# Kernel optimization log

Hardware: AMD Instinct MI355X
Metric: run time of the kernel (lower is better)

## Reference

```python
import jax, jax.numpy as jnp
import numpy as np

B, S, D_IN, D_H = 16, 4096, 512, 512

def setup_inputs() -> dict:
    key = jax.random.key(0)
    ks = jax.random.split(key, 8)
    inp = {
        "input": jax.random.normal(ks[0], (B, D_IN), dtype=jnp.float32),
        "context": jax.random.normal(ks[1], (B, S, D_IN), dtype=jnp.float32),
        "mask": jax.random.bernoulli(ks[2], 0.2, (B, S)),
        # parameters (torch nn.Linear layout: W [out,in], b [out])
        "W_in": jax.random.normal(ks[3], (D_H, D_IN), dtype=jnp.float32) / np.sqrt(D_IN),
        "b_in": jax.random.normal(ks[4], (D_H,), dtype=jnp.float32) * 0.01,
        "W_ctx": jax.random.normal(ks[5], (D_H, D_IN), dtype=jnp.float32) / np.sqrt(D_IN),
        "b_ctx": jax.random.normal(ks[6], (D_H,), dtype=jnp.float32) * 0.01,
        "v": jax.random.normal(ks[7], (D_H,), dtype=jnp.float32),
    }
    return inp


def reference(input, context, mask, W_in, b_in, W_ctx, b_ctx, v):
    # inp: [B, H] projected decoder state
    inp = input @ W_in.T + b_in
    # ctx: [B, S, H] projected context (this is what the torch code matmuls
    # with the softmax weights, i.e. hidden lives in hidden_dim space)
    ctx = context @ W_ctx.T + b_ctx
    # additive (Bahdanau) scores: v . tanh(inp + ctx) -> [B, S]
    scores = jnp.einsum("h,bsh->bs", v, jnp.tanh(inp[:, None, :] + ctx))
    # masked positions get -inf so they receive zero softmax weight
    scores = jnp.where(mask, -jnp.inf, scores)
    attn = jax.nn.softmax(scores, axis=-1)  # [B, S]
    # weighted sum of projected context: [B, H]
    hidden = jnp.einsum("bsh,bs->bh", ctx, attn)
    return hidden, attn
```

## Files before the change

kernel.cpp:

```cpp
#include <hip/hip_runtime.h>
#include <hip/hip_bf16.h>

#define B_  16
#define S_  4096
#define DIN 512
#define DH  512

typedef _Float16 f16x8 __attribute__((ext_vector_type(8)));
typedef float    f32x4 __attribute__((ext_vector_type(4)));


__device__ __forceinline__ float fast_tanh(float x) {
    float e = __expf(2.f * x);
    return 1.f - 2.f * __builtin_amdgcn_rcpf(e + 1.f);
}

__device__ __forceinline__ void gload_lds16(const void* g, void* l) {
    __builtin_amdgcn_global_load_lds(
        (const __attribute__((address_space(1))) void*)g,
        (__attribute__((address_space(3))) void*)l, 16, 0, 0);
}

__device__ __forceinline__ int mask_at(const void* mask, int isByte, int idx) {
    return isByte ? (int)((const unsigned char*)mask)[idx]
                  : ((const int*)mask)[idx];
}

__global__ __launch_bounds__(256)
void prep_kernel(const float* __restrict__ input,
                 const float* __restrict__ W_in,
                 const float* __restrict__ b_in,
                 const float* __restrict__ W_ctx,
                 const float* __restrict__ b_ctx,
                 const void*  __restrict__ mask,
                 _Float16* __restrict__ W16,
                 float* __restrict__ addv,
                 float* __restrict__ wsum,
                 int* __restrict__ maskflag) {
    int blk = blockIdx.x;
    int tid = threadIdx.x;
    if (blk < 256) {
        int base = blk * 1024 + tid * 4;
        float4 wv = *(const float4*)(W_ctx + base);
        union { _Float16 f[4]; ushort4 u; } cv;
        cv.f[0] = (_Float16)wv.x; cv.f[1] = (_Float16)wv.y;
        cv.f[2] = (_Float16)wv.z; cv.f[3] = (_Float16)wv.w;
        *(ushort4*)(W16 + base) = cv.u;
    } else if (blk < 288) {
        int t = blk - 256;
        int b = t >> 1;
        int h = ((t & 1) << 8) + tid;
        __shared__ float inrow[DIN];
        inrow[tid]       = input[b * DIN + tid];
        inrow[tid + 256] = input[b * DIN + tid + 256];
        __syncthreads();
        const float* wr = W_in + (size_t)h * DIN;
        float acc = 0.f;
        for (int k = 0; k < DIN; k += 4) {
            float4 w4 = *(const float4*)(wr + k);
            acc += w4.x * inrow[k] + w4.y * inrow[k + 1]
                 + w4.z * inrow[k + 2] + w4.w * inrow[k + 3];
        }
        addv[b * DH + h] = acc + b_in[h] + b_ctx[h];
    } else if (blk == 288) {
        const uint4* m4 = (const uint4*)mask;
        unsigned int orw = 0;
#pragma unroll
        for (int it = 0; it < 16; ++it) {
            uint4 w = m4[it * 256 + tid];
            orw |= (w.x | w.y | w.z | w.w);
        }
        int found = ((orw & 0xFFFFFF00u) != 0) ? 1 : 0;
        __shared__ int f;
        if (tid == 0) f = 0;
        __syncthreads();
        if (found) atomicOr(&f, 1);
        __syncthreads();
        if (tid == 0) maskflag[0] = f;
    } else {
        int base = (blk - 289) * 4096;
#pragma unroll
        for (int it = 0; it < 16; ++it)
            wsum[base + it * 256 + tid] = 0.f;
    }
}

__global__ __launch_bounds__(512, 1)
void score_kernel(const float* __restrict__ context,
                  const _Float16* __restrict__ W16,
                  const float* __restrict__ addv,
                  const float* __restrict__ v,
                  float* __restrict__ scores) {
    __shared__ __align__(16) _Float16 As[2][4096];
    __shared__ __align__(16) _Float16 Bs[2][16384];

    const int tid  = threadIdx.x;
    const int wave = tid >> 6;
    const int lane = tid & 63;
    const int l15  = lane & 15;
    const int q    = lane >> 4;
    const int sg   = wave >> 2;
    const int ng   = wave & 3;

    const int b  = blockIdx.x >> 5;
    const int st = blockIdx.x & 31;
    const int s0 = st * 128;

    const float* ctxA = context + ((size_t)b * S_ + s0) * DIN;

    const int rowA = ((tid >> 6) * 16) + (tid & 15);
    const int kbA  = ((tid >> 4) & 3) * 8;

#define STAGE_B(kc_, buf_)                                                     \
    {                                                                          \
        _Pragma("unroll")                                                      \
        for (int u = 0; u < 4; ++u) {                                          \
            int jn = wave * 4 + u;                                             \
            const _Float16* gp = W16 +                                         \
                (size_t)(jn * 16 + l15) * DIN + (kc_) * 32 + q * 8;            \
            gload_lds16(gp, &Bs[buf_][jn * 512]);                              \
        }                                                                      \
    }

#define LOADA(kc_, set_)                                                       \
    {                                                                          \
        const float* g0 = ctxA + (size_t)rowA * DIN + (kc_) * 32 + kbA;        \
        set_[0] = *(const float4*)g0;                                          \
        set_[1] = *(const float4*)(g0 + 4);                                    \
    }

#define WRITEA(set_, buf_)                                                     \
    {                                                                          \
        f16x8 h0;                                                              \
        h0[0] = (_Float16)set_[0].x; h0[1] = (_Float16)set_[0].y;              \
        h0[2] = (_Float16)set_[0].z; h0[3] = (_Float16)set_[0].w;              \
        h0[4] = (_Float16)set_[1].x; h0[5] = (_Float16)set_[1].y;              \
        h0[6] = (_Float16)set_[1].z; h0[7] = (_Float16)set_[1].w;              \
        *(f16x8*)&As[buf_][tid * 8] = h0;                                      \
    }

    f32x4 acc[4][8];
#pragma unroll
    for (int jm = 0; jm < 4; ++jm)
#pragma unroll
        for (int jn = 0; jn < 8; ++jn) acc[jm][jn] = (f32x4){0.f, 0.f, 0.f, 0.f};

    float4 aA[2], aB[2];

    STAGE_B(0, 0);
    LOADA(0, aA);
    WRITEA(aA, 0);
    LOADA(1, aB);
    __syncthreads();

#define STEP(kc_, buf_, ldset_, wrset_)                                        \
    {                                                                          \
        if ((kc_) + 1 < 16) STAGE_B((kc_) + 1, (buf_) ^ 1);                    \
        if ((kc_) + 2 < 16) LOADA((kc_) + 2, ldset_);                          \
        f16x8 afr[4], bfr[8];                                                  \
        _Pragma("unroll")                                                      \
        for (int jm = 0; jm < 4; ++jm)                                         \
            afr[jm] = *(const f16x8*)&As[buf_][(sg * 4 + jm) * 512 +           \
                                              q * 128 + l15 * 8];              \
        _Pragma("unroll")                                                      \
        for (int jn = 0; jn < 8; ++jn)                                         \
            bfr[jn] = *(const f16x8*)&Bs[buf_][(ng * 8 + jn) * 512 +           \
                                              q * 128 + l15 * 8];              \
        _Pragma("unroll")                                                      \
        for (int jn = 0; jn < 8; ++jn)                                         \
            _Pragma("unroll")                                                  \
            for (int jm = 0; jm < 4; ++jm)                                     \
                acc[jm][jn] = __builtin_amdgcn_mfma_f32_16x16x32_f16(          \
                    afr[jm], bfr[jn], acc[jm][jn], 0, 0, 0);                   \
        if ((kc_) + 1 < 16) WRITEA(wrset_, (buf_) ^ 1);                        \
        __syncthreads();                                                       \
    }

    for (int kp = 0; kp < 8; ++kp) {
        STEP(2 * kp,     0, aA, aB);
        STEP(2 * kp + 1, 1, aB, aA);
    }

    const float* avb = addv + b * DH;
    float rowsum[4][4] = {{0.f,0.f,0.f,0.f},{0.f,0.f,0.f,0.f},
                          {0.f,0.f,0.f,0.f},{0.f,0.f,0.f,0.f}};
#pragma unroll
    for (int jn = 0; jn < 8; ++jn) {
        int n = (ng * 8 + jn) * 16 + l15;
        float av = avb[n];
        float vv = v[n];
#pragma unroll
        for (int jm = 0; jm < 4; ++jm)
#pragma unroll
            for (int r = 0; r < 4; ++r)
                rowsum[jm][r] += vv * fast_tanh(acc[jm][jn][r] + av);
    }
    float* sredF = (float*)&As[0][0];
#pragma unroll
    for (int jm = 0; jm < 4; ++jm)
#pragma unroll
        for (int r = 0; r < 4; ++r) {
            float s = rowsum[jm][r];
            s += __shfl_xor(s, 1, 16);
            s += __shfl_xor(s, 2, 16);
            s += __shfl_xor(s, 4, 16);
            s += __shfl_xor(s, 8, 16);
            if (l15 == 0) {
                int rowL = (sg * 4 + jm) * 16 + q * 4 + r;
                sredF[ng * 128 + rowL] = s;
            }
        }
    __syncthreads();
    if (tid < 128) {
        float out = sredF[tid] + sredF[128 + tid] +
                    sredF[256 + tid] + sredF[384 + tid];
        scores[b * S_ + s0 + tid] = out;
    }
}

__global__ __launch_bounds__(256)
void attnwsum_kernel(const float* __restrict__ scores,
                     const float* __restrict__ context,
                     const void* __restrict__ mask,
                     const int* __restrict__ maskflag,
                     float* __restrict__ attn,
                     float* __restrict__ wsum) {
    __shared__ float rbuf[8];
    __shared__ int   selIdx[64];
    __shared__ float selW[64];
    __shared__ int   selCount;
    __shared__ float sh[1024];

    int b  = blockIdx.x >> 6;
    int c0 = (blockIdx.x & 63) * 64;
    int tid = threadIdx.x;
    int wv = tid >> 6, ln = tid & 63;
    int isByte = maskflag[0];
    const float* sr = scores + b * S_;

    float mx = -__builtin_inff();
    float vals[16];
#pragma unroll
    for (int it = 0; it < 16; ++it) {
        int s = it * 256 + tid;
        float x = mask_at(mask, isByte, b * S_ + s) ? -__builtin_inff() : sr[s];
        vals[it] = x;
        mx = fmaxf(mx, x);
    }
    for (int o = 1; o < 64; o <<= 1) mx = fmaxf(mx, __shfl_xor(mx, o, 64));
    if (ln == 0) rbuf[wv] = mx;
    __syncthreads();
    mx = fmaxf(fmaxf(rbuf[0], rbuf[1]), fmaxf(rbuf[2], rbuf[3]));

    float sum = 0.f;
#pragma unroll
    for (int it = 0; it < 16; ++it) sum += __expf(vals[it] - mx);
    for (int o = 1; o < 64; o <<= 1) sum += __shfl_xor(sum, o, 64);
    if (ln == 0) rbuf[4 + wv] = sum;
    if (tid == 0) selCount = 0;
    __syncthreads();
    float inv = 1.f / (rbuf[4] + rbuf[5] + rbuf[6] + rbuf[7]);

    if (tid < 64) {
        int s = c0 + tid;
        int idx = b * S_ + s;
        float sc = mask_at(mask, isByte, idx) ? -__builtin_inff() : sr[s];
        float p = __expf(sc - mx) * inv;
        attn[idx] = p;
        if (p > 1e-9f) {
            int k = atomicAdd(&selCount, 1);
            selIdx[k] = s;
            selW[k]  = p;
        }
    }
    __syncthreads();

    int cnt = selCount;
    if (cnt == 0) return;

    const float* cb = context + (size_t)b * S_ * DIN;
    const int p  = tid >> 7;
    const int hb = (tid & 127) * 4;
    float4 aE = {0.f, 0.f, 0.f, 0.f};
    float4 aO = {0.f, 0.f, 0.f, 0.f};
    int i = p;
    for (; i + 2 < cnt; i += 4) {
        const float* r0 = cb + (size_t)selIdx[i]     * DIN + hb;
        const float* r1 = cb + (size_t)selIdx[i + 2] * DIN + hb;
        float w0 = selW[i], w1 = selW[i + 2];
        float4 v0 = *(const float4*)r0;
        float4 v1 = *(const float4*)r1;
        aE.x += w0 * v0.x; aE.y += w0 * v0.y; aE.z += w0 * v0.z; aE.w += w0 * v0.w;
        aO.x += w1 * v1.x; aO.y += w1 * v1.y; aO.z += w1 * v1.z; aO.w += w1 * v1.w;
    }
    for (; i < cnt; i += 2) {
        const float* r0 = cb + (size_t)selIdx[i] * DIN + hb;
        float w0 = selW[i];
        float4 v0 = *(const float4*)r0;
        aE.x += w0 * v0.x; aE.y += w0 * v0.y; aE.z += w0 * v0.z; aE.w += w0 * v0.w;
    }
    aE.x += aO.x; aE.y += aO.y; aE.z += aO.z; aE.w += aO.w;
    *(float4*)&sh[p * 512 + hb] = aE;
    __syncthreads();

    {
        float v0 = sh[tid]       + sh[512 + tid];
        float v1 = sh[tid + 256] + sh[768 + tid];
        atomicAdd(&wsum[b * DIN + tid],       v0);
        atomicAdd(&wsum[b * DIN + tid + 256], v1);
    }
}

__global__ __launch_bounds__(256)
void hidden_kernel(const float* __restrict__ W_ctx,
                   const float* __restrict__ b_ctx,
                   const float* __restrict__ wsum,
                   float* __restrict__ hidden) {
    int b = blockIdx.x >> 1;
    int tid = threadIdx.x;
    int h = ((blockIdx.x & 1) << 8) + tid;
    __shared__ float wrow[DIN];
    wrow[tid]       = wsum[b * DIN + tid];
    wrow[tid + 256] = wsum[b * DIN + tid + 256];
    __syncthreads();
    const float* wr = W_ctx + (size_t)h * DIN;
    float acc = 0.f;
    for (int k = 0; k < DIN; k += 4) {
        float4 w4 = *(const float4*)(wr + k);
        acc += w4.x * wrow[k] + w4.y * wrow[k + 1]
             + w4.z * wrow[k + 2] + w4.w * wrow[k + 3];
    }
    hidden[b * DH + h] = acc + b_ctx[h];
}

extern "C" void kernel_launch(void* const* d_in, const int* in_sizes, int n_in,
                              void* d_out, int out_size, void* d_ws, size_t ws_size,
                              hipStream_t stream) {
    const float* input   = (const float*)d_in[0];
    const float* context = (const float*)d_in[1];
    const void*  mask    = d_in[2];
    const float* W_in    = (const float*)d_in[3];
    const float* b_in    = (const float*)d_in[4];
    const float* W_ctx   = (const float*)d_in[5];
    const float* b_ctx   = (const float*)d_in[6];
    const float* v       = (const float*)d_in[7];

    char* ws = (char*)d_ws;
    _Float16* W16   = (_Float16*)ws;
    float* addv     = (float*)(ws + 524288);
    float* scores   = (float*)(ws + 557056);
    float* wsum     = (float*)(ws + 819200);
    int*   maskflag = (int*)(ws + 851968);

    float* hidden = (float*)d_out;
    float* attn   = (float*)d_out + B_ * DH;

    prep_kernel<<<291, 256, 0, stream>>>(input, W_in, b_in, W_ctx, b_ctx, mask,
                                         W16, addv, wsum, maskflag);
    score_kernel<<<512, 512, 0, stream>>>(context, W16, addv, v, scores);
    attnwsum_kernel<<<B_ * 64, 256, 0, stream>>>(scores, context, mask, maskflag,
                                                 attn, wsum);
    hidden_kernel<<<B_ * 2, 256, 0, stream>>>(W_ctx, b_ctx, wsum, hidden);
}
```

Measured before the change: 292.1 us.

## Drop LDS staging in score kernel, load MFMA fragments directly from global

The score GEMM no longer stages the fp16 weights and converted context through double-buffered LDS. Each wave now loads its A and B fragments straight from global memory into registers with a two-deep register prefetch. The tile shrinks to 64 rows with each wave owning 64 output columns, which doubles the grid and drops the per-step block barriers. The trade-off is much less cross-wave reuse: each context row is read by all 8 waves and the weights are re-read by every block, so more traffic falls on L1/L2.

```diff
diff --git a/kernel.cpp b/kernel.cpp
--- a/kernel.cpp
+++ b/kernel.cpp
@@ -13,12 +13,6 @@
 __device__ __forceinline__ float fast_tanh(float x) {
     float e = __expf(2.f * x);
     return 1.f - 2.f * __builtin_amdgcn_rcpf(e + 1.f);
-}
-
-__device__ __forceinline__ void gload_lds16(const void* g, void* l) {
-    __builtin_amdgcn_global_load_lds(
-        (const __attribute__((address_space(1))) void*)g,
-        (__attribute__((address_space(3))) void*)l, 16, 0, 0);
 }
 
 __device__ __forceinline__ int mask_at(const void* mask, int isByte, int idx) {
@@ -85,108 +79,85 @@
     }
 }
 
-__global__ __launch_bounds__(512, 1)
+__global__ __launch_bounds__(512)
 void score_kernel(const float* __restrict__ context,
                   const _Float16* __restrict__ W16,
                   const float* __restrict__ addv,
                   const float* __restrict__ v,
                   float* __restrict__ scores) {
-    __shared__ __align__(16) _Float16 As[2][4096];
-    __shared__ __align__(16) _Float16 Bs[2][16384];
+    __shared__ float sred[8][64];
 
     const int tid  = threadIdx.x;
-    const int wave = tid >> 6;
+    const int ng   = tid >> 6;
     const int lane = tid & 63;
     const int l15  = lane & 15;
     const int q    = lane >> 4;
-    const int sg   = wave >> 2;
-    const int ng   = wave & 3;
-
-    const int b  = blockIdx.x >> 5;
-    const int st = blockIdx.x & 31;
-    const int s0 = st * 128;
-
-    const float* ctxA = context + ((size_t)b * S_ + s0) * DIN;
-
-    const int rowA = ((tid >> 6) * 16) + (tid & 15);
-    const int kbA  = ((tid >> 4) & 3) * 8;
-
-#define STAGE_B(kc_, buf_)                                                     \
+
+    const int b  = blockIdx.x >> 6;
+    const int st = blockIdx.x & 63;
+    const int s0 = st * 64;
+
+    const float*    ctxA = context + ((size_t)b * S_ + s0) * DIN;
+    const _Float16* Wn   = W16 + (size_t)(ng * 64) * DIN;
+
+    const int rbase = l15 * DIN + q * 8;
+
+#define LOADAB(kc_, as_, bs_)                                                  \
     {                                                                          \
         _Pragma("unroll")                                                      \
-        for (int u = 0; u < 4; ++u) {                                          \
-            int jn = wave * 4 + u;                                             \
-            const _Float16* gp = W16 +                                         \
-                (size_t)(jn * 16 + l15) * DIN + (kc_) * 32 + q * 8;            \
-            gload_lds16(gp, &Bs[buf_][jn * 512]);                              \
+        for (int jm = 0; jm < 4; ++jm) {                                       \
+            const float* g = ctxA + jm * 16 * DIN + rbase + (kc_) * 32;        \
+            as_[2 * jm]     = *(const float4*)g;                               \
+            as_[2 * jm + 1] = *(const float4*)(g + 4);                         \
         }                                                                      \
-    }
-
-#define LOADA(kc_, set_)                                                       \
+        _Pragma("unroll")                                                      \
+        for (int jn = 0; jn < 4; ++jn)                                         \
+            bs_[jn] = *(const f16x8*)(Wn + jn * 16 * DIN + rbase + (kc_) * 32);\
+    }
+
+#define CVTMFMA(as_, bs_)                                                      \
     {                                                                          \
-        const float* g0 = ctxA + (size_t)rowA * DIN + (kc_) * 32 + kbA;        \
-        set_[0] = *(const float4*)g0;                                          \
-        set_[1] = *(const float4*)(g0 + 4);                                    \
-    }
-
-#define WRITEA(set_, buf_)                                                     \
-    {                                                                          \
-        f16x8 h0;                                                              \
-        h0[0] = (_Float16)set_[0].x; h0[1] = (_Float16)set_[0].y;              \
-        h0[2] = (_Float16)set_[0].z; h0[3] = (_Float16)set_[0].w;              \
-        h0[4] = (_Float16)set_[1].x; h0[5] = (_Float16)set_[1].y;              \
-        h0[6] = (_Float16)set_[1].z; h0[7] = (_Float16)set_[1].w;              \
-        *(f16x8*)&As[buf_][tid * 8] = h0;                                      \
-    }
-
-    f32x4 acc[4][8];
-#pragma unroll
-    for (int jm = 0; jm < 4; ++jm)
-#pragma unroll
-        for (int jn = 0; jn < 8; ++jn) acc[jm][jn] = (f32x4){0.f, 0.f, 0.f, 0.f};
-
-    float4 aA[2], aB[2];
-
-    STAGE_B(0, 0);
-    LOADA(0, aA);
-    WRITEA(aA, 0);
-    LOADA(1, aB);
-    __syncthreads();
-
-#define STEP(kc_, buf_, ldset_, wrset_)                                        \
-    {                                                                          \
-        if ((kc_) + 1 < 16) STAGE_B((kc_) + 1, (buf_) ^ 1);                    \
-        if ((kc_) + 2 < 16) LOADA((kc_) + 2, ldset_);                          \
-        f16x8 afr[4], bfr[8];                                                  \
+        f16x8 afr[4];                                                          \
         _Pragma("unroll")                                                      \
-        for (int jm = 0; jm < 4; ++jm)                                         \
-            afr[jm] = *(const f16x8*)&As[buf_][(sg * 4 + jm) * 512 +           \
-                                              q * 128 + l15 * 8];              \
+        for (int jm = 0; jm < 4; ++jm) {                                       \
+            f16x8 t;                                                           \
+            t[0] = (_Float16)as_[2 * jm].x;  t[1] = (_Float16)as_[2 * jm].y;   \
+            t[2] = (_Float16)as_[2 * jm].z;  t[3] = (_Float16)as_[2 * jm].w;   \
+            t[4] = (_Float16)as_[2 * jm + 1].x; t[5] = (_Float16)as_[2 * jm + 1].y; \
+            t[6] = (_Float16)as_[2 * jm + 1].z; t[7] = (_Float16)as_[2 * jm + 1].w; \
+            afr[jm] = t;                                                       \
+        }                                                                      \
         _Pragma("unroll")                                                      \
-        for (int jn = 0; jn < 8; ++jn)                                         \
-            bfr[jn] = *(const f16x8*)&Bs[buf_][(ng * 8 + jn) * 512 +           \
-                                              q * 128 + l15 * 8];              \
-        _Pragma("unroll")                                                      \
-        for (int jn = 0; jn < 8; ++jn)                                         \
+        for (int jn = 0; jn < 4; ++jn)                                         \
             _Pragma("unroll")                                                  \
             for (int jm = 0; jm < 4; ++jm)                                     \
                 acc[jm][jn] = __builtin_amdgcn_mfma_f32_16x16x32_f16(          \
-                    afr[jm], bfr[jn], acc[jm][jn], 0, 0, 0);                   \
-        if ((kc_) + 1 < 16) WRITEA(wrset_, (buf_) ^ 1);                        \
-        __syncthreads();                                                       \
-    }
-
+                    afr[jm], bs_[jn], acc[jm][jn], 0, 0, 0);                   \
+    }
+
+    f32x4 acc[4][4];
+#pragma unroll
+    for (int jm = 0; jm < 4; ++jm)
+#pragma unroll
+        for (int jn = 0; jn < 4; ++jn) acc[jm][jn] = (f32x4){0.f, 0.f, 0.f, 0.f};
+
+    float4 aS0[8], aS1[8];
+    f16x8  bS0[4], bS1[4];
+
+    LOADAB(0, aS0, bS0);
     for (int kp = 0; kp < 8; ++kp) {
-        STEP(2 * kp,     0, aA, aB);
-        STEP(2 * kp + 1, 1, aB, aA);
+        LOADAB(2 * kp + 1, aS1, bS1);
+        CVTMFMA(aS0, bS0);
+        if (kp < 7) LOADAB(2 * kp + 2, aS0, bS0);
+        CVTMFMA(aS1, bS1);
     }
 
     const float* avb = addv + b * DH;
     float rowsum[4][4] = {{0.f,0.f,0.f,0.f},{0.f,0.f,0.f,0.f},
                           {0.f,0.f,0.f,0.f},{0.f,0.f,0.f,0.f}};
 #pragma unroll
-    for (int jn = 0; jn < 8; ++jn) {
-        int n = (ng * 8 + jn) * 16 + l15;
+    for (int jn = 0; jn < 4; ++jn) {
+        int n = ng * 64 + jn * 16 + l15;
         float av = avb[n];
         float vv = v[n];
 #pragma unroll
@@ -195,7 +166,6 @@
             for (int r = 0; r < 4; ++r)
                 rowsum[jm][r] += vv * fast_tanh(acc[jm][jn][r] + av);
     }
-    float* sredF = (float*)&As[0][0];
 #pragma unroll
     for (int jm = 0; jm < 4; ++jm)
 #pragma unroll
@@ -205,15 +175,14 @@
             s += __shfl_xor(s, 2, 16);
             s += __shfl_xor(s, 4, 16);
             s += __shfl_xor(s, 8, 16);
-            if (l15 == 0) {
-                int rowL = (sg * 4 + jm) * 16 + q * 4 + r;
-                sredF[ng * 128 + rowL] = s;
-            }
+            if (l15 == 0)
+                sred[ng][jm * 16 + q * 4 + r] = s;
         }
     __syncthreads();
-    if (tid < 128) {
-        float out = sredF[tid] + sredF[128 + tid] +
-                    sredF[256 + tid] + sredF[384 + tid];
+    if (tid < 64) {
+        float out = 0.f;
+#pragma unroll
+        for (int w = 0; w < 8; ++w) out += sred[w][tid];
         scores[b * S_ + s0 + tid] = out;
     }
 }
@@ -357,7 +326,7 @@
 
     prep_kernel<<<291, 256, 0, stream>>>(input, W_in, b_in, W_ctx, b_ctx, mask,
                                          W16, addv, wsum, maskflag);
-    score_kernel<<<512, 512, 0, stream>>>(context, W16, addv, v, scores);
+    score_kernel<<<1024, 512, 0, stream>>>(context, W16, addv, v, scores);
     attnwsum_kernel<<<B_ * 64, 256, 0, stream>>>(scores, context, mask, maskflag,
                                                  attn, wsum);
     hidden_kernel<<<B_ * 2, 256, 0, stream>>>(W_ctx, b_ctx, wsum, hidden);
```

New measurement: 404.4 us. +38.4%, slower.
